# Performance work log

Measured on AMD Instinct MI355X. Metric: run time of the kernel, lower is better.

The kernel has to match this reference:

```python
import jax, jax.numpy as jnp
import numpy as np


def _ln(x, g, b):
    m = jnp.mean(x, axis=-1, keepdims=True)
    v = jnp.mean((x - m) ** 2, axis=-1, keepdims=True)
    return (x - m) / jnp.sqrt(v + 1e-5) * g + b


def _lstm(x, h, c, wih, whh, bih, bhh):
    # torch.nn.LSTMCell gate order: i, f, g, o
    gates = x @ wih.T + bih + h @ whh.T + bhh
    i, f, g, o = jnp.split(gates, 4, axis=-1)
    c_new = jax.nn.sigmoid(f) * c + jax.nn.sigmoid(i) * jnp.tanh(g)
    h_new = jax.nn.sigmoid(o) * jnp.tanh(c_new)
    return h_new, c_new


def setup_inputs():
    key = jax.random.key(0)
    ks = iter(jax.random.split(key, 32))
    H, V, E, B = 1024, 32000, 2048 * 3 * 3, 256

    def w(shape, s=0.02):
        return jax.random.normal(next(ks), shape, jnp.float32) * s

    return dict(
        features=jax.random.normal(next(ks), (B, E), jnp.float32),
        fc1_w=w((H, E)), fc1_b=w((H,)),
        init_h_w=w((H, H)), init_h_b=w((H,)),
        init_c_w=w((H, H)), init_c_b=w((H,)),
        ln_h_g=jnp.ones((H,), jnp.float32), ln_h_b=jnp.zeros((H,), jnp.float32),
        ln_c_g=jnp.ones((H,), jnp.float32), ln_c_b=jnp.zeros((H,), jnp.float32),
        w_ih1=w((4 * H, H)), w_hh1=w((4 * H, H)), b_ih1=w((4 * H,)), b_hh1=w((4 * H,)),
        w_ih2=w((4 * H, H)), w_hh2=w((4 * H, H)), b_ih2=w((4 * H,)), b_hh2=w((4 * H,)),
        fc_w=w((V, H)), fc_b=w((V,)),
        embed_w=w((V, H)),
        totoken_w=w((V, 1)),
        max_length=15,
    )


def reference(features, fc1_w, fc1_b, init_h_w, init_h_b, init_c_w, init_c_b,
              ln_h_g, ln_h_b, ln_c_g, ln_c_b,
              w_ih1, w_hh1, b_ih1, b_hh1, w_ih2, w_hh2, b_ih2, b_hh2,
              fc_w, fc_b, embed_w, totoken_w, max_length):
    # Dropout(0.5) is identity in eval mode.
    B = features.shape[0]
    feat = jax.nn.relu(features @ fc1_w.T + fc1_b)                       # [B,H]
    h = _ln(jax.nn.relu(feat @ init_h_w.T + init_h_b), ln_h_g, ln_h_b)   # [B,H]
    c = _ln(jax.nn.relu(feat @ init_c_w.T + init_c_b), ln_c_g, ln_c_b)
    h1, c1 = _lstm(feat, h, c, w_ih1, w_hh1, b_ih1, b_hh1)
    h2, c2 = _lstm(h1, h, c, w_ih2, w_hh2, b_ih2, b_hh2)
    h3, c3 = _lstm(h2, h, c, w_ih2, w_hh2, b_ih2, b_hh2)
    pred = h3 @ fc_w.T + fc_b                                            # [B,V]
    idx = jnp.argmax(pred, axis=1)
    # torch: res_caption[:, 0] = totoken(idx)[0]  -> row 0 broadcast over batch
    col0 = jnp.broadcast_to(totoken_w[idx][0], (B,))
    word = embed_w[idx]                                                  # [B,H]

    def step(carry, _):
        h1, c1, h2, c2, h3, c3, word = carry
        h1n, c1n = _lstm(word,
                         _ln(h1, ln_h_g, ln_h_b) + h,
                         _ln(c1, ln_c_g, ln_c_b) + c,
                         w_ih1, w_hh1, b_ih1, b_hh1)
        h2n, c2n = _lstm(h1n, h2, c2, w_ih2, w_hh2, b_ih2, b_hh2)
        h3n, c3n = _lstm(h2n, h3, c3, w_ih2, w_hh2, b_ih2, b_hh2)
        pred = h3n @ fc_w.T + fc_b
        idx = jnp.argmax(pred, axis=1)
        col = jnp.broadcast_to(totoken_w[idx][0], (B,))
        return (h1n, c1n, h2n, c2n, h3n, c3n, embed_w[idx]), col

    _, cols = jax.lax.scan(step, (h1, c1, h2, c2, h3, c3, word), None,
                           length=max_length - 1)                        # [T-1,B]
    return jnp.concatenate([col0[None, :], cols], axis=0).T              # [B,T]
```

## Files before the change

kernel.cpp:

```cpp
#include <hip/hip_runtime.h>
#include <math.h>


#define HDIM 1024
#define VDIM 32000
#define EDIM 18432
#define BDIM 256
#define TSTEPS 15
#define FC_BLOCKS 512

__device__ inline float wave_sum(float v) {
#pragma unroll
  for (int off = 32; off; off >>= 1) v += __shfl_down(v, off, 64);
  return v;
}

template <int NT>
__device__ inline float block_allreduce_sum(float v, float* sm) {
  const int NW = NT / 64;
  int lane = threadIdx.x & 63, wave = threadIdx.x >> 6;
  v = wave_sum(v);
  if (lane == 0) sm[wave] = v;
  __syncthreads();
  float r = (threadIdx.x < NW) ? sm[threadIdx.x] : 0.f;
  if (wave == 0) {
    r = wave_sum(r);
    if (lane == 0) sm[0] = r;
  }
  __syncthreads();
  r = sm[0];
  __syncthreads();
  return r;
}

__global__ __launch_bounds__(256) void gemv_relu(
    const float* __restrict__ W, const float* __restrict__ x,
    const float* __restrict__ b, float* __restrict__ y, int K) {
  __shared__ float sm[4];
  int r = blockIdx.x;
  const float4* wr = (const float4*)(W + (size_t)r * K);
  const float4* xv = (const float4*)x;
  int nk = K >> 2;
  float s = 0.f;
  for (int k = threadIdx.x; k < nk; k += 256) {
    float4 a = wr[k], c = xv[k];
    s = fmaf(a.x, c.x, fmaf(a.y, c.y, fmaf(a.z, c.z, fmaf(a.w, c.w, s))));
  }
  s = block_allreduce_sum<256>(s, sm);
  if (threadIdx.x == 0) y[r] = fmaxf(s + b[r], 0.f);
}

__global__ __launch_bounds__(1024) void ln2_kernel(
    const float* __restrict__ ph, const float* __restrict__ pc,
    const float* __restrict__ gh, const float* __restrict__ bh,
    const float* __restrict__ gc, const float* __restrict__ bc,
    float* __restrict__ h, float* __restrict__ c) {
  __shared__ float sm[16];
  int t = threadIdx.x;
  float xh = ph[t];
  float m = block_allreduce_sum<1024>(xh, sm) * (1.f / 1024.f);
  float d = xh - m;
  float var = block_allreduce_sum<1024>(d * d, sm) * (1.f / 1024.f);
  h[t] = d / sqrtf(var + 1e-5f) * gh[t] + bh[t];
  float xc = pc[t];
  float mc = block_allreduce_sum<1024>(xc, sm) * (1.f / 1024.f);
  float dc = xc - mc;
  float vc = block_allreduce_sum<1024>(dc * dc, sm) * (1.f / 1024.f);
  c[t] = dc / sqrtf(vc + 1e-5f) * gc[t] + bc[t];
}

__global__ __launch_bounds__(256) void lstm_cell(
    const float* __restrict__ x, const float* __restrict__ hs,
    const float* __restrict__ cs, const float* __restrict__ Wih,
    const float* __restrict__ Whh, const float* __restrict__ bih,
    const float* __restrict__ bhh, float* __restrict__ hout,
    float* __restrict__ cout) {
  __shared__ float g[4];
  int j = blockIdx.x;
  int lane = threadIdx.x & 63, wave = threadIdx.x >> 6;
  size_t row = (size_t)(j + wave * HDIM);
  const float4* wi = (const float4*)(Wih + row * HDIM);
  const float4* wh = (const float4*)(Whh + row * HDIM);
  const float4* xv = (const float4*)x;
  const float4* hv = (const float4*)hs;
  float s = 0.f;
#pragma unroll
  for (int it = 0; it < 4; ++it) {
    int k = lane + (it << 6);
    float4 a = wi[k], c = xv[k];
    s = fmaf(a.x, c.x, fmaf(a.y, c.y, fmaf(a.z, c.z, fmaf(a.w, c.w, s))));
    float4 d = wh[k], e = hv[k];
    s = fmaf(d.x, e.x, fmaf(d.y, e.y, fmaf(d.z, e.z, fmaf(d.w, e.w, s))));
  }
  s = wave_sum(s);
  if (lane == 0) g[wave] = s + bih[row] + bhh[row];
  __syncthreads();
  if (threadIdx.x == 0) {
    float gi = g[0], gf = g[1], gg = g[2], go = g[3];
    float si = 1.f / (1.f + expf(-gi));
    float sf = 1.f / (1.f + expf(-gf));
    float so = 1.f / (1.f + expf(-go));
    float cn = sf * cs[j] + si * tanhf(gg);
    cout[j] = cn;
    hout[j] = so * tanhf(cn);
  }
}

__global__ __launch_bounds__(256) void fc_argmax_part(
    const float* __restrict__ W, const float* __restrict__ b,
    const float* __restrict__ x, float* __restrict__ bmax,
    int* __restrict__ bidx) {
  __shared__ float sv[4];
  __shared__ int sidx[4];
  int lane = threadIdx.x & 63, wave = threadIdx.x >> 6;
  int wid = blockIdx.x * 4 + wave;
  const float4* xv = (const float4*)x;
  float best = -3.4e38f;
  int bi = 0x7fffffff;
  for (int row = wid; row < VDIM; row += FC_BLOCKS * 4) {
    const float4* wr = (const float4*)(W + (size_t)row * HDIM);
    float s = 0.f;
#pragma unroll
    for (int it = 0; it < 4; ++it) {
      int k = lane + (it << 6);
      float4 a = wr[k], c = xv[k];
      s = fmaf(a.x, c.x, fmaf(a.y, c.y, fmaf(a.z, c.z, fmaf(a.w, c.w, s))));
    }
    s = wave_sum(s);
    if (lane == 0) {
      s += b[row];
      if (s > best) { best = s; bi = row; }
    }
  }
  if (lane == 0) { sv[wave] = best; sidx[wave] = bi; }
  __syncthreads();
  if (threadIdx.x == 0) {
    float v = sv[0];
    int ix = sidx[0];
#pragma unroll
    for (int w2 = 1; w2 < 4; ++w2) {
      if (sv[w2] > v || (sv[w2] == v && sidx[w2] < ix)) { v = sv[w2]; ix = sidx[w2]; }
    }
    bmax[blockIdx.x] = v;
    bidx[blockIdx.x] = ix;
  }
}

__global__ __launch_bounds__(512) void finalize(
    const float* __restrict__ bmax, const int* __restrict__ bidx,
    const float* __restrict__ totoken, const float* __restrict__ embed,
    const float* __restrict__ h1, const float* __restrict__ c1,
    const float* __restrict__ h0, const float* __restrict__ c0,
    const float* __restrict__ gh, const float* __restrict__ bh,
    const float* __restrict__ gc, const float* __restrict__ bc,
    float* __restrict__ word, float* __restrict__ x1h, float* __restrict__ x1c,
    float* __restrict__ out, int step) {
  __shared__ float sm[8];
  __shared__ int smi[8];
  __shared__ int s_idx;
  int t = threadIdx.x, lane = t & 63, wave = t >> 6;
  float v = bmax[t];
  int ix = bidx[t];
#pragma unroll
  for (int off = 32; off; off >>= 1) {
    float ov = __shfl_down(v, off, 64);
    int oi = __shfl_down(ix, off, 64);
    if (ov > v || (ov == v && oi < ix)) { v = ov; ix = oi; }
  }
  if (lane == 0) { sm[wave] = v; smi[wave] = ix; }
  __syncthreads();
  if (t == 0) {
    float bv = sm[0];
    int bi = smi[0];
#pragma unroll
    for (int w2 = 1; w2 < 8; ++w2) {
      if (sm[w2] > bv || (sm[w2] == bv && smi[w2] < bi)) { bv = sm[w2]; bi = smi[w2]; }
    }
    s_idx = bi;
  }
  __syncthreads();
  int idx = s_idx;
  float tv = totoken[idx];
  if (t < BDIM) out[t * TSTEPS + step] = tv;
  for (int k = t; k < HDIM; k += 512) word[k] = embed[(size_t)idx * HDIM + k];
  __syncthreads();
  float a0 = h1[t], a1 = h1[t + 512];
  float m = block_allreduce_sum<512>(a0 + a1, sm) * (1.f / 1024.f);
  float d0 = a0 - m, d1 = a1 - m;
  float var = block_allreduce_sum<512>(d0 * d0 + d1 * d1, sm) * (1.f / 1024.f);
  float inv = 1.f / sqrtf(var + 1e-5f);
  x1h[t] = d0 * inv * gh[t] + bh[t] + h0[t];
  x1h[t + 512] = d1 * inv * gh[t + 512] + bh[t + 512] + h0[t + 512];
  float b0 = c1[t], b1 = c1[t + 512];
  float mc = block_allreduce_sum<512>(b0 + b1, sm) * (1.f / 1024.f);
  float e0 = b0 - mc, e1 = b1 - mc;
  float vc = block_allreduce_sum<512>(e0 * e0 + e1 * e1, sm) * (1.f / 1024.f);
  float invc = 1.f / sqrtf(vc + 1e-5f);
  x1c[t] = e0 * invc * gc[t] + bc[t] + c0[t];
  x1c[t + 512] = e1 * invc * gc[t + 512] + bc[t + 512] + c0[t + 512];
}

extern "C" void kernel_launch(void* const* d_in, const int* in_sizes, int n_in,
                              void* d_out, int out_size, void* d_ws,
                              size_t ws_size, hipStream_t stream) {
  (void)in_sizes; (void)n_in; (void)out_size; (void)ws_size;
  const float* features = (const float*)d_in[0];
  const float* fc1_w    = (const float*)d_in[1];
  const float* fc1_b    = (const float*)d_in[2];
  const float* init_h_w = (const float*)d_in[3];
  const float* init_h_b = (const float*)d_in[4];
  const float* init_c_w = (const float*)d_in[5];
  const float* init_c_b = (const float*)d_in[6];
  const float* ln_h_g   = (const float*)d_in[7];
  const float* ln_h_b   = (const float*)d_in[8];
  const float* ln_c_g   = (const float*)d_in[9];
  const float* ln_c_b   = (const float*)d_in[10];
  const float* w_ih1    = (const float*)d_in[11];
  const float* w_hh1    = (const float*)d_in[12];
  const float* b_ih1    = (const float*)d_in[13];
  const float* b_hh1    = (const float*)d_in[14];
  const float* w_ih2    = (const float*)d_in[15];
  const float* w_hh2    = (const float*)d_in[16];
  const float* b_ih2    = (const float*)d_in[17];
  const float* b_hh2    = (const float*)d_in[18];
  const float* fc_w     = (const float*)d_in[19];
  const float* fc_b     = (const float*)d_in[20];
  const float* embed_w  = (const float*)d_in[21];
  const float* totoken  = (const float*)d_in[22];

  float* ws = (float*)d_ws;
  float* feat = ws + 0;
  float* preh = ws + 1024;
  float* prec = ws + 2048;
  float* h0   = ws + 3072;
  float* c0   = ws + 4096;
  float* h1   = ws + 5120;
  float* c1   = ws + 6144;
  float* h2b[2] = {ws + 7168, ws + 8192};
  float* c2b[2] = {ws + 9216, ws + 10240};
  float* h3b[2] = {ws + 11264, ws + 12288};
  float* c3b[2] = {ws + 13312, ws + 14336};
  float* x1h  = ws + 15360;
  float* x1c  = ws + 16384;
  float* word = ws + 17408;
  float* bmax = ws + 18432;
  int*   bidx = (int*)(ws + 18432 + FC_BLOCKS);
  float* out  = (float*)d_out;

  gemv_relu<<<HDIM, 256, 0, stream>>>(fc1_w, features, fc1_b, feat, EDIM);
  gemv_relu<<<HDIM, 256, 0, stream>>>(init_h_w, feat, init_h_b, preh, HDIM);
  gemv_relu<<<HDIM, 256, 0, stream>>>(init_c_w, feat, init_c_b, prec, HDIM);
  ln2_kernel<<<1, 1024, 0, stream>>>(preh, prec, ln_h_g, ln_h_b, ln_c_g, ln_c_b,
                                     h0, c0);
  lstm_cell<<<HDIM, 256, 0, stream>>>(feat, h0, c0, w_ih1, w_hh1, b_ih1, b_hh1,
                                      h1, c1);
  lstm_cell<<<HDIM, 256, 0, stream>>>(h1, h0, c0, w_ih2, w_hh2, b_ih2, b_hh2,
                                      h2b[0], c2b[0]);
  lstm_cell<<<HDIM, 256, 0, stream>>>(h2b[0], h0, c0, w_ih2, w_hh2, b_ih2,
                                      b_hh2, h3b[0], c3b[0]);
  fc_argmax_part<<<FC_BLOCKS, 256, 0, stream>>>(fc_w, fc_b, h3b[0], bmax, bidx);
  finalize<<<1, 512, 0, stream>>>(bmax, bidx, totoken, embed_w, h1, c1, h0, c0,
                                  ln_h_g, ln_h_b, ln_c_g, ln_c_b, word, x1h,
                                  x1c, out, 0);
  int cur = 0;
  for (int t = 1; t < TSTEPS; ++t) {
    int nxt = cur ^ 1;
    lstm_cell<<<HDIM, 256, 0, stream>>>(word, x1h, x1c, w_ih1, w_hh1, b_ih1,
                                        b_hh1, h1, c1);
    lstm_cell<<<HDIM, 256, 0, stream>>>(h1, h2b[cur], c2b[cur], w_ih2, w_hh2,
                                        b_ih2, b_hh2, h2b[nxt], c2b[nxt]);
    lstm_cell<<<HDIM, 256, 0, stream>>>(h2b[nxt], h3b[cur], c3b[cur], w_ih2,
                                        w_hh2, b_ih2, b_hh2, h3b[nxt],
                                        c3b[nxt]);
    fc_argmax_part<<<FC_BLOCKS, 256, 0, stream>>>(fc_w, fc_b, h3b[nxt], bmax,
                                                  bidx);
    finalize<<<1, 512, 0, stream>>>(bmax, bidx, totoken, embed_w, h1, c1, h0,
                                    c0, ln_h_g, ln_h_b, ln_c_g, ln_c_b, word,
                                    x1h, x1c, out, t);
    cur = nxt;
  }
}
```

Before: 1.080 ms.

## Convert LSTM and vocab weights to fp16 and fuse argmax finalize via last-block counter

Result: slower. 1.138 ms (+5.3%).

```diff
diff --git a/kernel.cpp b/kernel.cpp
--- a/kernel.cpp
+++ b/kernel.cpp
@@ -1,4 +1,5 @@
 #include <hip/hip_runtime.h>
+#include <hip/hip_fp16.h>
 #include <math.h>
 
 
@@ -31,6 +32,26 @@
   r = sm[0];
   __syncthreads();
   return r;
+}
+
+__global__ __launch_bounds__(256) void f2h8(const float* __restrict__ src,
+                                            __half* __restrict__ dst, int n8) {
+  int i = blockIdx.x * 256 + threadIdx.x;
+  int stride = gridDim.x * 256;
+  const float4* s = (const float4*)src;
+  for (; i < n8; i += stride) {
+    float4 a = s[2 * i], b = s[2 * i + 1];
+    __half2 hh[4];
+    hh[0] = __floats2half2_rn(a.x, a.y);
+    hh[1] = __floats2half2_rn(a.z, a.w);
+    hh[2] = __floats2half2_rn(b.x, b.y);
+    hh[3] = __floats2half2_rn(b.z, b.w);
+    ((float4*)dst)[i] = *(float4*)hh;
+  }
+}
+
+__global__ void zero_counters(int* c) {
+  if (threadIdx.x < 32) c[threadIdx.x] = 0;
 }
 
 __global__ __launch_bounds__(256) void gemv_relu(
@@ -69,10 +90,10 @@
   c[t] = dc / sqrtf(vc + 1e-5f) * gc[t] + bc[t];
 }
 
-__global__ __launch_bounds__(256) void lstm_cell(
+__global__ __launch_bounds__(256) void lstm_cell_h(
     const float* __restrict__ x, const float* __restrict__ hs,
-    const float* __restrict__ cs, const float* __restrict__ Wih,
-    const float* __restrict__ Whh, const float* __restrict__ bih,
+    const float* __restrict__ cs, const __half* __restrict__ Wih,
+    const __half* __restrict__ Whh, const float* __restrict__ bih,
     const float* __restrict__ bhh, float* __restrict__ hout,
     float* __restrict__ cout) {
   __shared__ float g[4];
@@ -85,12 +106,22 @@
   const float4* hv = (const float4*)hs;
   float s = 0.f;
 #pragma unroll
-  for (int it = 0; it < 4; ++it) {
+  for (int it = 0; it < 2; ++it) {
     int k = lane + (it << 6);
-    float4 a = wi[k], c = xv[k];
-    s = fmaf(a.x, c.x, fmaf(a.y, c.y, fmaf(a.z, c.z, fmaf(a.w, c.w, s))));
-    float4 d = wh[k], e = hv[k];
-    s = fmaf(d.x, e.x, fmaf(d.y, e.y, fmaf(d.z, e.z, fmaf(d.w, e.w, s))));
+    float4 wa = wi[k], wb = wh[k];
+    float4 x0 = xv[2 * k], x1 = xv[2 * k + 1];
+    float4 h0 = hv[2 * k], h1 = hv[2 * k + 1];
+    const __half2* A = (const __half2*)&wa;
+    const __half2* B = (const __half2*)&wb;
+    float2 f;
+    f = __half22float2(A[0]); s = fmaf(f.x, x0.x, fmaf(f.y, x0.y, s));
+    f = __half22float2(A[1]); s = fmaf(f.x, x0.z, fmaf(f.y, x0.w, s));
+    f = __half22float2(A[2]); s = fmaf(f.x, x1.x, fmaf(f.y, x1.y, s));
+    f = __half22float2(A[3]); s = fmaf(f.x, x1.z, fmaf(f.y, x1.w, s));
+    f = __half22float2(B[0]); s = fmaf(f.x, h0.x, fmaf(f.y, h0.y, s));
+    f = __half22float2(B[1]); s = fmaf(f.x, h0.z, fmaf(f.y, h0.w, s));
+    f = __half22float2(B[2]); s = fmaf(f.x, h1.x, fmaf(f.y, h1.y, s));
+    f = __half22float2(B[3]); s = fmaf(f.x, h1.z, fmaf(f.y, h1.w, s));
   }
   s = wave_sum(s);
   if (lane == 0) g[wave] = s + bih[row] + bhh[row];
@@ -106,13 +137,22 @@
   }
 }
 
-__global__ __launch_bounds__(256) void fc_argmax_part(
-    const float* __restrict__ W, const float* __restrict__ b,
+__global__ __launch_bounds__(256) void fc_argmax_fin(
+    const __half* __restrict__ W, const float* __restrict__ b,
     const float* __restrict__ x, float* __restrict__ bmax,
-    int* __restrict__ bidx) {
+    int* __restrict__ bidx, int* __restrict__ counter,
+    const float* __restrict__ totoken, const float* __restrict__ embed,
+    const float* __restrict__ h1, const float* __restrict__ c1,
+    const float* __restrict__ h0v, const float* __restrict__ c0v,
+    const float* __restrict__ gh, const float* __restrict__ bh,
+    const float* __restrict__ gc, const float* __restrict__ bc,
+    float* __restrict__ word, float* __restrict__ x1h, float* __restrict__ x1c,
+    float* __restrict__ out, int step) {
   __shared__ float sv[4];
   __shared__ int sidx[4];
-  int lane = threadIdx.x & 63, wave = threadIdx.x >> 6;
+  __shared__ int s_last;
+  __shared__ int s_idx;
+  int t = threadIdx.x, lane = t & 63, wave = t >> 6;
   int wid = blockIdx.x * 4 + wave;
   const float4* xv = (const float4*)x;
   float best = -3.4e38f;
@@ -121,10 +161,16 @@
     const float4* wr = (const float4*)(W + (size_t)row * HDIM);
     float s = 0.f;
 #pragma unroll
-    for (int it = 0; it < 4; ++it) {
+    for (int it = 0; it < 2; ++it) {
       int k = lane + (it << 6);
-      float4 a = wr[k], c = xv[k];
-      s = fmaf(a.x, c.x, fmaf(a.y, c.y, fmaf(a.z, c.z, fmaf(a.w, c.w, s))));
+      float4 wa = wr[k];
+      float4 x0 = xv[2 * k], x1 = xv[2 * k + 1];
+      const __half2* A = (const __half2*)&wa;
+      float2 f;
+      f = __half22float2(A[0]); s = fmaf(f.x, x0.x, fmaf(f.y, x0.y, s));
+      f = __half22float2(A[1]); s = fmaf(f.x, x0.z, fmaf(f.y, x0.w, s));
+      f = __half22float2(A[2]); s = fmaf(f.x, x1.x, fmaf(f.y, x1.y, s));
+      f = __half22float2(A[3]); s = fmaf(f.x, x1.z, fmaf(f.y, x1.w, s));
     }
     s = wave_sum(s);
     if (lane == 0) {
@@ -134,7 +180,7 @@
   }
   if (lane == 0) { sv[wave] = best; sidx[wave] = bi; }
   __syncthreads();
-  if (threadIdx.x == 0) {
+  if (t == 0) {
     float v = sv[0];
     int ix = sidx[0];
 #pragma unroll
@@ -143,61 +189,59 @@
     }
     bmax[blockIdx.x] = v;
     bidx[blockIdx.x] = ix;
-  }
-}
-
-__global__ __launch_bounds__(512) void finalize(
-    const float* __restrict__ bmax, const int* __restrict__ bidx,
-    const float* __restrict__ totoken, const float* __restrict__ embed,
-    const float* __restrict__ h1, const float* __restrict__ c1,
-    const float* __restrict__ h0, const float* __restrict__ c0,
-    const float* __restrict__ gh, const float* __restrict__ bh,
-    const float* __restrict__ gc, const float* __restrict__ bc,
-    float* __restrict__ word, float* __restrict__ x1h, float* __restrict__ x1c,
-    float* __restrict__ out, int step) {
-  __shared__ float sm[8];
-  __shared__ int smi[8];
-  __shared__ int s_idx;
-  int t = threadIdx.x, lane = t & 63, wave = t >> 6;
-  float v = bmax[t];
-  int ix = bidx[t];
+    __threadfence();
+    int old = atomicAdd(counter, 1);
+    s_last = (old == FC_BLOCKS - 1) ? 1 : 0;
+  }
+  __syncthreads();
+  if (!s_last) return;
+  __threadfence();
+  float v0 = bmax[t];       int i0 = bidx[t];
+  float v1 = bmax[t + 256]; int i1 = bidx[t + 256];
+  if (v1 > v0 || (v1 == v0 && i1 < i0)) { v0 = v1; i0 = i1; }
 #pragma unroll
   for (int off = 32; off; off >>= 1) {
-    float ov = __shfl_down(v, off, 64);
-    int oi = __shfl_down(ix, off, 64);
-    if (ov > v || (ov == v && oi < ix)) { v = ov; ix = oi; }
-  }
-  if (lane == 0) { sm[wave] = v; smi[wave] = ix; }
+    float ov = __shfl_down(v0, off, 64);
+    int oi = __shfl_down(i0, off, 64);
+    if (ov > v0 || (ov == v0 && oi < i0)) { v0 = ov; i0 = oi; }
+  }
+  if (lane == 0) { sv[wave] = v0; sidx[wave] = i0; }
   __syncthreads();
   if (t == 0) {
-    float bv = sm[0];
-    int bi = smi[0];
-#pragma unroll
-    for (int w2 = 1; w2 < 8; ++w2) {
-      if (sm[w2] > bv || (sm[w2] == bv && smi[w2] < bi)) { bv = sm[w2]; bi = smi[w2]; }
+    float bv = sv[0];
+    int bix = sidx[0];
+#pragma unroll
+    for (int w2 = 1; w2 < 4; ++w2) {
+      if (sv[w2] > bv || (sv[w2] == bv && sidx[w2] < bix)) { bv = sv[w2]; bix = sidx[w2]; }
     }
-    s_idx = bi;
+    s_idx = bix;
   }
   __syncthreads();
   int idx = s_idx;
   float tv = totoken[idx];
-  if (t < BDIM) out[t * TSTEPS + step] = tv;
-  for (int k = t; k < HDIM; k += 512) word[k] = embed[(size_t)idx * HDIM + k];
-  __syncthreads();
-  float a0 = h1[t], a1 = h1[t + 512];
-  float m = block_allreduce_sum<512>(a0 + a1, sm) * (1.f / 1024.f);
-  float d0 = a0 - m, d1 = a1 - m;
-  float var = block_allreduce_sum<512>(d0 * d0 + d1 * d1, sm) * (1.f / 1024.f);
+  out[t * TSTEPS + step] = tv;
+  for (int k = t; k < HDIM; k += 256) word[k] = embed[(size_t)idx * HDIM + k];
+  __syncthreads();
+  float a0 = h1[t], a1 = h1[t + 256], a2 = h1[t + 512], a3 = h1[t + 768];
+  float m = block_allreduce_sum<256>(a0 + a1 + a2 + a3, sv) * (1.f / 1024.f);
+  float d0 = a0 - m, d1 = a1 - m, d2 = a2 - m, d3 = a3 - m;
+  float var = block_allreduce_sum<256>(d0 * d0 + d1 * d1 + d2 * d2 + d3 * d3, sv) *
+              (1.f / 1024.f);
   float inv = 1.f / sqrtf(var + 1e-5f);
-  x1h[t] = d0 * inv * gh[t] + bh[t] + h0[t];
-  x1h[t + 512] = d1 * inv * gh[t + 512] + bh[t + 512] + h0[t + 512];
-  float b0 = c1[t], b1 = c1[t + 512];
-  float mc = block_allreduce_sum<512>(b0 + b1, sm) * (1.f / 1024.f);
-  float e0 = b0 - mc, e1 = b1 - mc;
-  float vc = block_allreduce_sum<512>(e0 * e0 + e1 * e1, sm) * (1.f / 1024.f);
+  x1h[t]       = d0 * inv * gh[t]       + bh[t]       + h0v[t];
+  x1h[t + 256] = d1 * inv * gh[t + 256] + bh[t + 256] + h0v[t + 256];
+  x1h[t + 512] = d2 * inv * gh[t + 512] + bh[t + 512] + h0v[t + 512];
+  x1h[t + 768] = d3 * inv * gh[t + 768] + bh[t + 768] + h0v[t + 768];
+  float b0 = c1[t], b1 = c1[t + 256], b2 = c1[t + 512], b3 = c1[t + 768];
+  float mc = block_allreduce_sum<256>(b0 + b1 + b2 + b3, sv) * (1.f / 1024.f);
+  float e0 = b0 - mc, e1 = b1 - mc, e2 = b2 - mc, e3 = b3 - mc;
+  float vc = block_allreduce_sum<256>(e0 * e0 + e1 * e1 + e2 * e2 + e3 * e3, sv) *
+             (1.f / 1024.f);
   float invc = 1.f / sqrtf(vc + 1e-5f);
-  x1c[t] = e0 * invc * gc[t] + bc[t] + c0[t];
-  x1c[t + 512] = e1 * invc * gc[t + 512] + bc[t + 512] + c0[t + 512];
+  x1c[t]       = e0 * invc * gc[t]       + bc[t]       + c0v[t];
+  x1c[t + 256] = e1 * invc * gc[t + 256] + bc[t + 256] + c0v[t + 256];
+  x1c[t + 512] = e2 * invc * gc[t + 512] + bc[t + 512] + c0v[t + 512];
+  x1c[t + 768] = e3 * invc * gc[t + 768] + bc[t + 768] + c0v[t + 768];
 }
 
 extern "C" void kernel_launch(void* const* d_in, const int* in_sizes, int n_in,
@@ -244,39 +288,51 @@
   float* x1c  = ws + 16384;
   float* word = ws + 17408;
   float* bmax = ws + 18432;
-  int*   bidx = (int*)(ws + 18432 + FC_BLOCKS);
+  int*   bidx = (int*)(ws + 18944);
+  int*   counters = (int*)(ws + 19456);
   float* out  = (float*)d_out;
+
+  __half* hb   = (__half*)((char*)d_ws + (1 << 17));
+  __half* fc_h = hb;
+  __half* w1i_h = hb + (size_t)32768 * 1024;
+  __half* w1h_h = w1i_h + (size_t)4 * 1024 * 1024;
+  __half* w2i_h = w1h_h + (size_t)4 * 1024 * 1024;
+  __half* w2h_h = w2i_h + (size_t)4 * 1024 * 1024;
+
+  zero_counters<<<1, 64, 0, stream>>>(counters);
+  f2h8<<<2048, 256, 0, stream>>>(fc_w,  fc_h,  (VDIM * HDIM) / 8);
+  f2h8<<<512, 256, 0, stream>>>(w_ih1, w1i_h, (4 * HDIM * HDIM) / 8);
+  f2h8<<<512, 256, 0, stream>>>(w_hh1, w1h_h, (4 * HDIM * HDIM) / 8);
+  f2h8<<<512, 256, 0, stream>>>(w_ih2, w2i_h, (4 * HDIM * HDIM) / 8);
+  f2h8<<<512, 256, 0, stream>>>(w_hh2, w2h_h, (4 * HDIM * HDIM) / 8);
 
   gemv_relu<<<HDIM, 256, 0, stream>>>(fc1_w, features, fc1_b, feat, EDIM);
   gemv_relu<<<HDIM, 256, 0, stream>>>(init_h_w, feat, init_h_b, preh, HDIM);
   gemv_relu<<<HDIM, 256, 0, stream>>>(init_c_w, feat, init_c_b, prec, HDIM);
   ln2_kernel<<<1, 1024, 0, stream>>>(preh, prec, ln_h_g, ln_h_b, ln_c_g, ln_c_b,
                                      h0, c0);
-  lstm_cell<<<HDIM, 256, 0, stream>>>(feat, h0, c0, w_ih1, w_hh1, b_ih1, b_hh1,
-                                      h1, c1);
-  lstm_cell<<<HDIM, 256, 0, stream>>>(h1, h0, c0, w_ih2, w_hh2, b_ih2, b_hh2,
-                                      h2b[0], c2b[0]);
-  lstm_cell<<<HDIM, 256, 0, stream>>>(h2b[0], h0, c0, w_ih2, w_hh2, b_ih2,
-                                      b_hh2, h3b[0], c3b[0]);
-  fc_argmax_part<<<FC_BLOCKS, 256, 0, stream>>>(fc_w, fc_b, h3b[0], bmax, bidx);
-  finalize<<<1, 512, 0, stream>>>(bmax, bidx, totoken, embed_w, h1, c1, h0, c0,
-                                  ln_h_g, ln_h_b, ln_c_g, ln_c_b, word, x1h,
-                                  x1c, out, 0);
+  lstm_cell_h<<<HDIM, 256, 0, stream>>>(feat, h0, c0, w1i_h, w1h_h, b_ih1,
+                                        b_hh1, h1, c1);
+  lstm_cell_h<<<HDIM, 256, 0, stream>>>(h1, h0, c0, w2i_h, w2h_h, b_ih2, b_hh2,
+                                        h2b[0], c2b[0]);
+  lstm_cell_h<<<HDIM, 256, 0, stream>>>(h2b[0], h0, c0, w2i_h, w2h_h, b_ih2,
+                                        b_hh2, h3b[0], c3b[0]);
+  fc_argmax_fin<<<FC_BLOCKS, 256, 0, stream>>>(
+      fc_h, fc_b, h3b[0], bmax, bidx, counters + 0, totoken, embed_w, h1, c1,
+      h0, c0, ln_h_g, ln_h_b, ln_c_g, ln_c_b, word, x1h, x1c, out, 0);
   int cur = 0;
   for (int t = 1; t < TSTEPS; ++t) {
     int nxt = cur ^ 1;
-    lstm_cell<<<HDIM, 256, 0, stream>>>(word, x1h, x1c, w_ih1, w_hh1, b_ih1,
-                                        b_hh1, h1, c1);
-    lstm_cell<<<HDIM, 256, 0, stream>>>(h1, h2b[cur], c2b[cur], w_ih2, w_hh2,
-                                        b_ih2, b_hh2, h2b[nxt], c2b[nxt]);
-    lstm_cell<<<HDIM, 256, 0, stream>>>(h2b[nxt], h3b[cur], c3b[cur], w_ih2,
-                                        w_hh2, b_ih2, b_hh2, h3b[nxt],
-                                        c3b[nxt]);
-    fc_argmax_part<<<FC_BLOCKS, 256, 0, stream>>>(fc_w, fc_b, h3b[nxt], bmax,
-                                                  bidx);
-    finalize<<<1, 512, 0, stream>>>(bmax, bidx, totoken, embed_w, h1, c1, h0,
-                                    c0, ln_h_g, ln_h_b, ln_c_g, ln_c_b, word,
-                                    x1h, x1c, out, t);
+    lstm_cell_h<<<HDIM, 256, 0, stream>>>(word, x1h, x1c, w1i_h, w1h_h, b_ih1,
+                                          b_hh1, h1, c1);
+    lstm_cell_h<<<HDIM, 256, 0, stream>>>(h1, h2b[cur], c2b[cur], w2i_h, w2h_h,
+                                          b_ih2, b_hh2, h2b[nxt], c2b[nxt]);
+    lstm_cell_h<<<HDIM, 256, 0, stream>>>(h2b[nxt], h3b[cur], c3b[cur], w2i_h,
+                                          w2h_h, b_ih2, b_hh2, h3b[nxt],
+                                          c3b[nxt]);
+    fc_argmax_fin<<<FC_BLOCKS, 256, 0, stream>>>(
+        fc_h, fc_b, h3b[nxt], bmax, bidx, counters + t, totoken, embed_w, h1,
+        c1, h0, c0, ln_h_g, ln_h_b, ln_c_g, ln_c_b, word, x1h, x1c, out, t);
     cur = nxt;
   }
 }
```
